# Performance work log

Measured on AMD Instinct MI355X. Metric: run time of the kernel, lower is better.

Reference implementation:

```python
import jax, jax.numpy as jnp
import numpy as np

EPS = 1e-5
NUM_HEADS = 8

def _inorm(x):
    # InstanceNorm1d (affine=False): normalize over last (length) axis per (B, C)
    m = x.mean(axis=-1, keepdims=True)
    v = x.var(axis=-1, keepdims=True)  # biased variance, as torch instance norm
    return (x - m) * jax.lax.rsqrt(v + EPS)

def setup_inputs() -> dict:
    key = jax.random.key(0)
    ks = jax.random.split(key, 12)
    B, Nl, HW = 4, 1024, 4096
    Cl, Cv, Ck, Cval, Cout = 512, 512, 256, 256, 256
    w = lambda k, shape: (jax.random.normal(k, shape, jnp.float32) * 0.02)
    return {
        "l": jax.random.normal(ks[0], (B, Nl, Cl), jnp.float32),
        "x": jax.random.normal(ks[1], (B, HW, Cv), jnp.float32),
        "Wq": w(ks[2], (Ck, Cl)),   "bq": w(ks[3], (Ck,)),
        "Wk": w(ks[4], (Ck, Cv)),   "bk": w(ks[5], (Ck,)),
        "Wv": w(ks[6], (Cval, Cv)), "bv": w(ks[7], (Cval,)),
        "Ww": w(ks[8], (Cout, Cval)), "bw": w(ks[9], (Cout,)),
    }

def reference(l, x, Wq, bq, Wk, bk, Wv, bv, Ww, bw):
    H = NUM_HEADS
    Ck = Wq.shape[0]
    Cv = Wv.shape[0]
    dk, dv = Ck // H, Cv // H
    B, Nl, _ = l.shape
    HW = x.shape[1]

    # 1x1 Conv1d == per-position linear
    q = jnp.einsum('blc,kc->blk', l, Wq) + bq                     # [B, Nl, Ck]
    k = jnp.einsum('bnc,kc->bkn', x, Wk) + bk[None, :, None]      # [B, Ck, HW]
    k = _inorm(k)                                                  # InstanceNorm over HW
    v = jnp.einsum('bnc,kc->bkn', x, Wv) + bv[None, :, None]      # [B, Cv, HW]

    q = q.reshape(B, Nl, H, dk).transpose(0, 2, 1, 3)             # [B, H, Nl, dk]
    k = k.reshape(B, H, dk, HW)                                   # [B, H, dk, HW]
    v = v.reshape(B, H, dv, HW)                                   # [B, H, dv, HW]

    sim = jnp.einsum('bhld,bhdn->bhln', q, k) * (Ck ** -0.5)      # [B, H, Nl, HW]
    att = jax.nn.softmax(sim, axis=-1)
    out = jnp.einsum('bhln,bhdn->bhld', att, v)                   # [B, H, Nl, dv]

    out = out.transpose(0, 2, 1, 3).reshape(B, Nl, Cv)            # [B, Nl, Cv]
    out = jnp.einsum('blc,oc->bol', out, Ww) + bw[None, :, None]  # [B, Cout, Nl]
    out = _inorm(out)                                              # InstanceNorm over Nl
    return out.transpose(0, 2, 1)                                  # [B, Nl, Cout]
```

## Files before the change

kernel.cpp:

```cpp
#include <hip/hip_runtime.h>

constexpr int Bn = 4, NL = 1024, HWn = 4096, NH = 8;

typedef __attribute__((ext_vector_type(8))) short bf16x8;
typedef __attribute__((ext_vector_type(4))) float f32x4;
#define MFMA16 __builtin_amdgcn_mfma_f32_16x16x32_bf16

extern "C" __device__ float __ocml_native_exp2_f32(float);

__device__ __forceinline__ float b2f(unsigned short u) {
  union { unsigned int i; float f; } x; x.i = ((unsigned int)u) << 16; return x.f;
}
__device__ __forceinline__ unsigned short f2b(float f) {
  union { float f; unsigned int i; } x; x.f = f;
  unsigned int r = x.i + 0x7fffu + ((x.i >> 16) & 1u);
  return (unsigned short)(r >> 16);
}

__global__ __launch_bounds__(256) void conv_bf16(const float* __restrict__ src,
    unsigned short* __restrict__ dst, int n)
{
  int i = (blockIdx.x * 256 + threadIdx.x) * 4;
  if (i < n) {
    float4 v = *(const float4*)(src + i);
    ushort4 o; o.x = f2b(v.x); o.y = f2b(v.y); o.z = f2b(v.z); o.w = f2b(v.w);
    *(ushort4*)(dst + i) = o;
  }
}

__global__ __launch_bounds__(256) void conv_w4(const float* __restrict__ Wk,
    const float* __restrict__ Wv, const float* __restrict__ Wq,
    const float* __restrict__ Ww,
    unsigned short* __restrict__ wkb, unsigned short* __restrict__ wvb,
    unsigned short* __restrict__ wqb,
    unsigned short* __restrict__ wwh, unsigned short* __restrict__ wwl)
{
  int i = (blockIdx.x * 256 + threadIdx.x) * 4;
  if (blockIdx.y == 3) {
    if (i >= 65536) return;
    float4 v = *(const float4*)(Ww + i);
    ushort4 hi, lo;
    hi.x = f2b(v.x); lo.x = f2b(v.x - b2f(hi.x));
    hi.y = f2b(v.y); lo.y = f2b(v.y - b2f(hi.y));
    hi.z = f2b(v.z); lo.z = f2b(v.z - b2f(hi.z));
    hi.w = f2b(v.w); lo.w = f2b(v.w - b2f(hi.w));
    *(ushort4*)(wwh + i) = hi;
    *(ushort4*)(wwl + i) = lo;
    return;
  }
  const float* src = blockIdx.y == 0 ? Wk : (blockIdx.y == 1 ? Wv : Wq);
  unsigned short* dst = blockIdx.y == 0 ? wkb : (blockIdx.y == 1 ? wvb : wqb);
  float4 v = *(const float4*)(src + i);
  ushort4 o; o.x = f2b(v.x); o.y = f2b(v.y); o.z = f2b(v.z); o.w = f2b(v.w);
  *(ushort4*)(dst + i) = o;
}

__global__ __launch_bounds__(256, 2) void gemm128(
    const unsigned short* __restrict__ xbf, const unsigned short* __restrict__ lbf,
    const unsigned short* __restrict__ wkb, const unsigned short* __restrict__ wvb,
    const unsigned short* __restrict__ wqb,
    const float* __restrict__ bk, const float* __restrict__ bv, const float* __restrict__ bq,
    unsigned short* __restrict__ khb, unsigned short* __restrict__ vhb,
    unsigned short* __restrict__ qbuf)
{
  __shared__ unsigned short As[2][128 * 32];
  __shared__ unsigned short Bs[2][128 * 32];
  const int id = blockIdx.x;
  const int mode = id < 256 ? 0 : (id < 512 ? 1 : 2);
  const int local = id - (mode == 0 ? 0 : (mode == 1 ? 256 : 512));
  const int rb = local >> 1, cb = local & 1;
  const int m0 = rb * 128, n0 = cb * 128;
  const unsigned short* A = (mode == 2) ? lbf : xbf;
  const unsigned short* W = (mode == 0) ? wkb : (mode == 1 ? wvb : wqb);
  const float* bias = (mode == 0) ? bk : (mode == 1 ? bv : bq);

  const int tid = threadIdx.x, w = tid >> 6, lane = tid & 63;
  const int quad = lane >> 4, l15 = lane & 15;
  const int wr = w >> 1, wc = w & 1;

  const int p0 = tid, p1 = tid + 256;
  const int am0 = p0 >> 2, ak0 = (p0 & 3) * 8;
  const int am1 = p1 >> 2, ak1 = (p1 & 3) * 8;

  f32x4 acc[4][4];
#pragma unroll
  for (int i = 0; i < 4; ++i)
#pragma unroll
    for (int j = 0; j < 4; ++j) acc[i][j] = (f32x4){0.f, 0.f, 0.f, 0.f};

  bf16x8 ar0 = *(const bf16x8*)(A + (size_t)(m0 + am0) * 512 + ak0);
  bf16x8 ar1 = *(const bf16x8*)(A + (size_t)(m0 + am1) * 512 + ak1);
  bf16x8 br0 = *(const bf16x8*)(W + (size_t)(n0 + am0) * 512 + ak0);
  bf16x8 br1 = *(const bf16x8*)(W + (size_t)(n0 + am1) * 512 + ak1);

  for (int kt = 0; kt < 16; ++kt) {
    const int cur = kt & 1;
    *(bf16x8*)&As[cur][p0 * 8] = ar0;
    *(bf16x8*)&As[cur][p1 * 8] = ar1;
    *(bf16x8*)&Bs[cur][p0 * 8] = br0;
    *(bf16x8*)&Bs[cur][p1 * 8] = br1;
    __syncthreads();
    if (kt < 15) {
      int k0 = (kt + 1) * 32;
      ar0 = *(const bf16x8*)(A + (size_t)(m0 + am0) * 512 + k0 + ak0);
      ar1 = *(const bf16x8*)(A + (size_t)(m0 + am1) * 512 + k0 + ak1);
      br0 = *(const bf16x8*)(W + (size_t)(n0 + am0) * 512 + k0 + ak0);
      br1 = *(const bf16x8*)(W + (size_t)(n0 + am1) * 512 + k0 + ak1);
    }
    bf16x8 af[4], bf[4];
#pragma unroll
    for (int fr = 0; fr < 4; ++fr)
      af[fr] = *(const bf16x8*)&As[cur][(wr * 64 + fr * 16 + l15) * 32 + quad * 8];
#pragma unroll
    for (int fc = 0; fc < 4; ++fc)
      bf[fc] = *(const bf16x8*)&Bs[cur][(wc * 64 + fc * 16 + l15) * 32 + quad * 8];
#pragma unroll
    for (int fr = 0; fr < 4; ++fr)
#pragma unroll
      for (int fc = 0; fc < 4; ++fc)
        acc[fr][fc] = MFMA16(af[fr], bf[fc], acc[fr][fc], 0, 0, 0);
  }

  float bb[4];
#pragma unroll
  for (int fc = 0; fc < 4; ++fc) bb[fc] = bias[n0 + wc * 64 + fc * 16 + l15];
  unsigned short* dst = (mode == 0) ? khb : (mode == 1 ? vhb : qbuf);
#pragma unroll
  for (int fr = 0; fr < 4; ++fr) {
#pragma unroll
    for (int fc = 0; fc < 4; ++fc) {
      int col = n0 + wc * 64 + fc * 16 + l15;
#pragma unroll
      for (int r = 0; r < 4; ++r) {
        int row = m0 + wr * 64 + fr * 16 + quad * 4 + r;
        unsigned short val = f2b(acc[fr][fc][r] + bb[fc]);
        if (mode == 2) {
          dst[(size_t)row * 256 + col] = val;
        } else {
          int b = row >> 12, n = row & 4095, h = col >> 5, d = col & 31;
          dst[((size_t)(b * 8 + h) * 4096 + n) * 32 + d] = val;
        }
      }
    }
  }
}

__global__ __launch_bounds__(256) void kvstats(const unsigned short* __restrict__ khb,
    const unsigned short* __restrict__ vhb,
    float* __restrict__ ksum, float* __restrict__ kss, float* __restrict__ vcs)
{
  const int which = blockIdx.x >> 5, bh = blockIdx.x & 31, seg = blockIdx.y;
  const int t = threadIdx.x, d = t & 31, g = t >> 5;
  __shared__ float rs[256], rss[256];
  if (which == 0) {
    const unsigned short* base = khb + (size_t)bh * 131072 + (size_t)seg * 512 * 32;
    float s = 0.f, ss = 0.f;
    for (int i = 0; i < 64; ++i) {
      float v = b2f(base[(size_t)(g + i * 8) * 32 + d]);
      s += v; ss += v * v;
    }
    rs[t] = s; rss[t] = ss;
    __syncthreads();
    if (t < 32) {
      float a = 0.f, b = 0.f;
      for (int g2 = 0; g2 < 8; ++g2) { a += rs[t + g2 * 32]; b += rss[t + g2 * 32]; }
      atomicAdd(&ksum[bh * 32 + t], a);
      atomicAdd(&kss[bh * 32 + t], b);
    }
  } else {
    const unsigned short* base = vhb + (size_t)bh * 131072 + (size_t)seg * 512 * 32;
    float s = 0.f;
    for (int i = 0; i < 64; ++i) s += b2f(base[(size_t)(g + i * 8) * 32 + d]);
    rs[t] = s;
    __syncthreads();
    if (t < 32) {
      float a = 0.f;
      for (int g2 = 0; g2 < 8; ++g2) a += rs[t + g2 * 32];
      vcs[seg * 1024 + bh * 32 + t] = a;
    }
  }
}

__global__ __launch_bounds__(256) void kfinal(const float* __restrict__ ksum,
    const float* __restrict__ kss, float* __restrict__ krstd)
{
  int i = blockIdx.x * 256 + threadIdx.x;
  float m = ksum[i] * (1.f / 4096.f);
  float var = kss[i] * (1.f / 4096.f) - m * m;
  krstd[i] = rsqrtf(var + 1e-5f);
}

__global__ __launch_bounds__(256) void vpack(const unsigned short* __restrict__ vh,
    unsigned short* __restrict__ vfrag)
{
  __shared__ unsigned short vt[256][42];
  const int bh = blockIdx.x >> 4, slab = blockIdx.x & 15;
  const unsigned short* src = vh + ((size_t)bh * 4096 + slab * 256) * 32;
  const int t = threadIdx.x;
#pragma unroll
  for (int i = 0; i < 4; ++i) {
    int p = i * 256 + t;
    int n = p >> 2, piece = p & 3;
    uint4 v = *(const uint4*)(src + (size_t)n * 32 + piece * 8);
    unsigned int* lrow = (unsigned int*)&vt[n][piece * 8];
    lrow[0] = v.x; lrow[1] = v.y; lrow[2] = v.z; lrow[3] = v.w;
  }
  __syncthreads();
#pragma unroll
  for (int i = 0; i < 4; ++i) {
    int op = i * 256 + t;
    int lanep = op & 63, rest = op >> 6;
    int dvt = rest & 1, kh2 = (rest >> 1) & 1, chunkl = rest >> 2;
    int lq = lanep >> 4, ll = lanep & 15;
    unsigned short o[8];
#pragma unroll
    for (int j = 0; j < 8; ++j) {
      int kappa = kh2 * 32 + lq * 8 + j;
      int nloc = (kappa >> 2) + 16 * (kappa & 3);
      o[j] = vt[chunkl * 64 + nloc][dvt * 16 + ll];
    }
    size_t dst = ((((size_t)bh * 64 + slab * 4 + chunkl) * 2 + kh2) * 2 + dvt) * 512 + lanep * 8;
    *(bf16x8*)(vfrag + dst) = *(const bf16x8*)o;
  }
}

__global__ __launch_bounds__(256, 2) void attn5(const unsigned short* __restrict__ qbuf,
    const unsigned short* __restrict__ khb, const unsigned short* __restrict__ vfrag,
    const float* __restrict__ krstd, const float* __restrict__ vcs,
    float* __restrict__ po, float* __restrict__ pd)
{
  const int bh = blockIdx.x, b = bh >> 3, h = bh & 7;
  const int lsuper = blockIdx.y, quarter = blockIdx.z;
  const int tid = threadIdx.x, w = tid >> 6, lane = tid & 63;
  const int quad = lane >> 4, l15 = lane & 15;

  __shared__ unsigned short kb_s[2][2048];
  __shared__ unsigned short vb_s[2][2048];
  __shared__ unsigned short ps[4][4][16][72];

  bf16x8 qa[4];
  {
    float fold[8];
    const float* rp = krstd + bh * 32 + quad * 8;
#pragma unroll
    for (int j = 0; j < 8; ++j) fold[j] = rp[j] * (0.0625f * 1.44269504f);
#pragma unroll
    for (int lf = 0; lf < 4; ++lf) {
      int l = lsuper * 256 + w * 64 + lf * 16 + l15;
      bf16x8 qr = *(const bf16x8*)(qbuf + ((size_t)(b * NL + l)) * 256 + h * 32 + quad * 8);
      const unsigned short* qq = (const unsigned short*)&qr;
      unsigned short tmp[8];
#pragma unroll
      for (int j = 0; j < 8; ++j) tmp[j] = f2b(b2f(qq[j]) * fold[j]);
      qa[lf] = *(const bf16x8*)tmp;
    }
  }

  float drow[4][4];
  f32x4 acc[4][2];
#pragma unroll
  for (int lf = 0; lf < 4; ++lf) {
#pragma unroll
    for (int r = 0; r < 4; ++r) drow[lf][r] = 0.f;
    acc[lf][0] = (f32x4){0.f,0.f,0.f,0.f};
    acc[lf][1] = (f32x4){0.f,0.f,0.f,0.f};
  }

  const unsigned short* kcbase = khb + (size_t)bh * 131072 + (size_t)quarter * 1024 * 32;
  const unsigned short* vcbase = vfrag + (size_t)bh * 131072 + (size_t)quarter * 16 * 2048;

  bf16x8 kreg = *(const bf16x8*)(kcbase + tid * 8);
  bf16x8 vreg = *(const bf16x8*)(vcbase + tid * 8);

  for (int c = 0; c < 16; ++c) {
    const int cur = c & 1;
    *(bf16x8*)&kb_s[cur][tid * 8] = kreg;
    *(bf16x8*)&vb_s[cur][tid * 8] = vreg;
    __syncthreads();
    if (c < 15) {
      kreg = *(const bf16x8*)(kcbase + (c + 1) * 2048 + tid * 8);
      vreg = *(const bf16x8*)(vcbase + (c + 1) * 2048 + tid * 8);
    }

    bf16x8 kb[4];
#pragma unroll
    for (int t = 0; t < 4; ++t)
      kb[t] = *(const bf16x8*)&kb_s[cur][(t * 16 + l15) * 32 + quad * 8];
    bf16x8 vb[4];
#pragma unroll
    for (int i = 0; i < 4; ++i)
      vb[i] = *(const bf16x8*)&vb_s[cur][i * 512 + lane * 8];

    f32x4 z = (f32x4){0.f,0.f,0.f,0.f};
#pragma unroll
    for (int lf = 0; lf < 4; ++lf) {
      f32x4 sv[4];
#pragma unroll
      for (int t = 0; t < 4; ++t) sv[t] = MFMA16(qa[lf], kb[t], z, 0, 0, 0);
#pragma unroll
      for (int r = 0; r < 4; ++r) {
        union { float f; unsigned int u; } e0, e1, e2, e3;
        float x0 = __ocml_native_exp2_f32(sv[0][r]);
        float x1 = __ocml_native_exp2_f32(sv[1][r]);
        float x2 = __ocml_native_exp2_f32(sv[2][r]);
        float x3 = __ocml_native_exp2_f32(sv[3][r]);
        drow[lf][r] += (x0 + x1) + (x2 + x3);
        e0.f = x0 - 1.0f; e1.f = x1 - 1.0f; e2.f = x2 - 1.0f; e3.f = x3 - 1.0f;
        unsigned int lo = (e0.u >> 16) | (e1.u & 0xFFFF0000u);
        unsigned int hi = (e2.u >> 16) | (e3.u & 0xFFFF0000u);
        unsigned int* dst = (unsigned int*)&ps[w][lf][quad * 4 + r][l15 * 4];
        dst[0] = lo; dst[1] = hi;
      }
      asm volatile("s_waitcnt lgkmcnt(0)" ::: "memory");
#pragma unroll
      for (int kh2 = 0; kh2 < 2; ++kh2) {
        bf16x8 pa = *(const bf16x8*)&ps[w][lf][l15][kh2 * 32 + quad * 8];
#pragma unroll
        for (int dvt = 0; dvt < 2; ++dvt)
          acc[lf][dvt] = MFMA16(pa, vb[kh2 * 2 + dvt], acc[lf][dvt], 0, 0, 0);
      }
    }
  }

  const float* vc0 = vcs + (quarter * 2) * 1024 + bh * 32;
  const float* vc1 = vc0 + 1024;
  float cs0 = vc0[l15] + vc1[l15];
  float cs1 = vc0[16 + l15] + vc1[16 + l15];
#pragma unroll
  for (int lf = 0; lf < 4; ++lf)
#pragma unroll
    for (int r = 0; r < 4; ++r) {
      acc[lf][0][r] += cs0;
      acc[lf][1][r] += cs1;
    }

  const size_t PDo = (size_t)quarter * 32768 + (size_t)bh * 1024;
#pragma unroll
  for (int lf = 0; lf < 4; ++lf) {
#pragma unroll
    for (int r = 0; r < 4; ++r) {
      float sv = drow[lf][r];
      sv += __shfl_xor(sv, 1, 16);
      sv += __shfl_xor(sv, 2, 16);
      sv += __shfl_xor(sv, 4, 16);
      sv += __shfl_xor(sv, 8, 16);
      int l = lsuper * 256 + w * 64 + lf * 16 + quad * 4 + r;
      float2 val; val.x = acc[lf][0][r]; val.y = acc[lf][1][r];
      *(float2*)(po + (PDo + l) * 32 + l15 * 2) = val;
      if (l15 == 0) pd[PDo + l] = sv;
    }
  }
}

__global__ __launch_bounds__(256) void combine4(const float* __restrict__ po,
    const float* __restrict__ pd, unsigned short* __restrict__ aoh,
    unsigned short* __restrict__ aol)
{
  int gid = blockIdx.x * 256 + threadIdx.x;
  int dv = gid & 31, l = (gid >> 5) & (NL - 1), h = (gid >> 15) & 7, b = gid >> 18;
  int c = ((dv & 15) << 1) | (dv >> 4);
  size_t r = ((size_t)(b * 8 + h)) * 1024 + l;
  float d = 0.f, o = 0.f;
#pragma unroll
  for (int q = 0; q < 4; ++q) {
    size_t rr = (size_t)q * 32768 + r;
    d += pd[rr];
    o += po[rr * 32 + c];
  }
  o = o / d;
  unsigned short hi = f2b(o);
  size_t idx = ((size_t)(b * NL) + l) * 256 + h * 32 + dv;
  aoh[idx] = hi;
  aol[idx] = f2b(o - b2f(hi));
}

__global__ __launch_bounds__(256) void gemm_proj(
    const unsigned short* __restrict__ aoh, const unsigned short* __restrict__ aol,
    const unsigned short* __restrict__ wwh, const unsigned short* __restrict__ wwl,
    const float* __restrict__ bw, float* __restrict__ pj)
{
  __shared__ unsigned short As[64 * 32];
  __shared__ unsigned short Bs[128 * 32];
  const int bm = blockIdx.x * 64, bn = blockIdx.y * 128;
  const int tid = threadIdx.x, w = tid >> 6, lane = tid & 63;
  const int quad = lane >> 4, l15 = lane & 15;
  const int wr = w >> 1, wc = w & 1;
  const int arow = tid >> 2, apiece = (tid & 3) * 8;

  f32x4 acc[2][4];
#pragma unroll
  for (int i = 0; i < 2; ++i)
#pragma unroll
    for (int j = 0; j < 4; ++j) acc[i][j] = (f32x4){0.f, 0.f, 0.f, 0.f};

  for (int pair = 0; pair < 3; ++pair) {
    const unsigned short* A = (pair == 1) ? aol : aoh;
    const unsigned short* Bm = (pair == 2) ? wwl : wwh;
    for (int kt = 0; kt < 8; ++kt) {
      int k0 = kt * 32;
      __syncthreads();
      *(bf16x8*)&As[tid * 8] = *(const bf16x8*)(A + (size_t)(bm + arow) * 256 + k0 + apiece);
#pragma unroll
      for (int it = 0; it < 2; ++it) {
        int p = tid + it * 256;
        int brow = p >> 2, bpiece = (p & 3) * 8;
        *(bf16x8*)&Bs[p * 8] = *(const bf16x8*)(Bm + (size_t)(bn + brow) * 256 + k0 + bpiece);
      }
      __syncthreads();
      bf16x8 af[2], bf[4];
#pragma unroll
      for (int fr = 0; fr < 2; ++fr)
        af[fr] = *(const bf16x8*)&As[(wr * 32 + fr * 16 + l15) * 32 + quad * 8];
#pragma unroll
      for (int fc = 0; fc < 4; ++fc)
        bf[fc] = *(const bf16x8*)&Bs[(wc * 64 + fc * 16 + l15) * 32 + quad * 8];
#pragma unroll
      for (int fr = 0; fr < 2; ++fr)
#pragma unroll
        for (int fc = 0; fc < 4; ++fc)
          acc[fr][fc] = MFMA16(af[fr], bf[fc], acc[fr][fc], 0, 0, 0);
    }
  }

#pragma unroll
  for (int fr = 0; fr < 2; ++fr)
#pragma unroll
    for (int fc = 0; fc < 4; ++fc) {
      int col = bn + wc * 64 + fc * 16 + l15;
      float bb = bw[col];
#pragma unroll
      for (int r = 0; r < 4; ++r) {
        int row = bm + wr * 32 + fr * 16 + quad * 4 + r;
        pj[(size_t)row * 256 + col] = acc[fr][fc][r] + bb;
      }
    }
}

__global__ __launch_bounds__(256) void stats_kernel(const float* __restrict__ X,
    long batchStride, int rowsPerBlock,
    float* __restrict__ sum, float* __restrict__ sumsq)
{
  const int b = blockIdx.x, c = threadIdx.x;
  const long r0 = (long)blockIdx.y * rowsPerBlock;
  const float* base = X + (long)b * batchStride + r0 * 256 + c;
  float s = 0.f, ss = 0.f;
  for (int r = 0; r < rowsPerBlock; ++r) {
    float v = base[(long)r * 256];
    s += v; ss += v * v;
  }
  atomicAdd(&sum[b * 256 + c], s);
  atomicAdd(&sumsq[b * 256 + c], ss);
}

__global__ __launch_bounds__(256) void finalize_stats(const float* __restrict__ sum,
    const float* __restrict__ sumsq, float invR,
    float* __restrict__ mean, float* __restrict__ rstd)
{
  int i = blockIdx.x * 256 + threadIdx.x;
  float m = sum[i] * invR;
  float v = sumsq[i] * invR - m * m;
  mean[i] = m;
  rstd[i] = rsqrtf(v + 1e-5f);
}

__global__ __launch_bounds__(256) void final_out(const float* __restrict__ proj,
    const float* __restrict__ mean, const float* __restrict__ rstd,
    float* __restrict__ out)
{
  const int b = blockIdx.x, o = threadIdx.x;
  const int l1 = blockIdx.y * 16;
  const float m = mean[b * 256 + o], r = rstd[b * 256 + o];
  for (int i = 0; i < 16; ++i) {
    size_t idx = ((size_t)(b * NL + l1 + i)) * 256 + o;
    out[idx] = (proj[idx] - m) * r;
  }
}

extern "C" void kernel_launch(void* const* d_in, const int* in_sizes, int n_in,
                              void* d_out, int out_size, void* d_ws, size_t ws_size,
                              hipStream_t stream)
{
  const float* l  = (const float*)d_in[0];
  const float* x  = (const float*)d_in[1];
  const float* Wq = (const float*)d_in[2];
  const float* bq = (const float*)d_in[3];
  const float* Wk = (const float*)d_in[4];
  const float* bk = (const float*)d_in[5];
  const float* Wv = (const float*)d_in[6];
  const float* bv = (const float*)d_in[7];
  const float* Ww = (const float*)d_in[8];
  const float* bw = (const float*)d_in[9];
  float* out = (float*)d_out;

  unsigned short* up = (unsigned short*)d_ws;
  unsigned short* xbf   = up;
  unsigned short* lbf   = xbf   + 8388608;
  unsigned short* wkb   = lbf   + 2097152;
  unsigned short* wvb   = wkb   + 131072;
  unsigned short* wqb   = wvb   + 131072;
  unsigned short* qbuf  = wqb   + 131072;
  unsigned short* khb   = qbuf  + 1048576;
  unsigned short* vhb   = khb   + 4194304;
  unsigned short* vfrag = vhb   + 4194304;
  unsigned short* aoh   = vfrag + 4194304;
  unsigned short* aol   = aoh   + 1048576;
  unsigned short* wwh   = aol   + 1048576;
  unsigned short* wwl   = wwh   + 65536;
  float* F     = (float*)((char*)d_ws + 53477376);
  float* krstd = F;
  float* vcs   = krstd + 1024;
  float* po    = vcs + 8192;
  float* pd    = po + 4194304;
  float* pj    = pd + 131072;
  float* st    = pj + 1048576;
  float* ksum  = st;          float* kss   = st + 1024;
  float* psum  = st + 2048;   float* psq   = st + 3072;
  float* pmean = st + 4096;   float* prstd = st + 5120;

  hipMemsetAsync(st, 0, 4096 * sizeof(float), stream);

  dim3 blk(256);
  conv_bf16<<<8192, blk, 0, stream>>>(x,  xbf, 8388608);
  conv_bf16<<<2048, blk, 0, stream>>>(l,  lbf, 2097152);
  conv_w4<<<dim3(128, 4), blk, 0, stream>>>(Wk, Wv, Wq, Ww, wkb, wvb, wqb, wwh, wwl);
  gemm128<<<576, blk, 0, stream>>>(xbf, lbf, wkb, wvb, wqb, bk, bv, bq, khb, vhb, qbuf);
  kvstats<<<dim3(64, 8), blk, 0, stream>>>(khb, vhb, ksum, kss, vcs);
  kfinal<<<4, blk, 0, stream>>>(ksum, kss, krstd);
  vpack<<<512, blk, 0, stream>>>(vhb, vfrag);
  attn5<<<dim3(32, 4, 4), blk, 0, stream>>>(qbuf, khb, vfrag, krstd, vcs, po, pd);
  combine4<<<4096, blk, 0, stream>>>(po, pd, aoh, aol);
  gemm_proj<<<dim3(64, 2), blk, 0, stream>>>(aoh, aol, wwh, wwl, bw, pj);
  stats_kernel<<<dim3(4, 64), blk, 0, stream>>>(pj, (long)NL * 256, 16, psum, psq);
  finalize_stats<<<4, blk, 0, stream>>>(psum, psq, 1.0f / NL, pmean, prstd);
  final_out<<<dim3(4, 64), blk, 0, stream>>>(pj, pmean, prstd, out);
}
```

Baseline: 204.3 us.

## Use direct global-to-LDS async loads and halve attention rows per block

Replaces register-staged global loads plus LDS stores with global_load_lds async copies in both the QKV GEMM and attention kernels. The attention kernel now covers 32 query rows per wave instead of 64, launching twice as many blocks with fewer registers, and occupancy hints are raised. This aims to cut VGPR pressure and LDS store instructions and to improve latency hiding. In exchange, each K/V tile is reloaded by twice as many blocks. There is also no explicit vmcnt wait before the barrier, so correctness depends on the compiler inserting one.

Result: no change. 203.7 us (-0.3%).

```diff
diff --git a/kernel.cpp b/kernel.cpp
--- a/kernel.cpp
+++ b/kernel.cpp
@@ -15,6 +15,12 @@
   union { float f; unsigned int i; } x; x.f = f;
   unsigned int r = x.i + 0x7fffu + ((x.i >> 16) & 1u);
   return (unsigned short)(r >> 16);
+}
+
+__device__ __forceinline__ void async_load16(const unsigned short* g, unsigned short* l) {
+  __builtin_amdgcn_global_load_lds(
+      (const __attribute__((address_space(1))) unsigned int*)g,
+      (__attribute__((address_space(3))) unsigned int*)l, 16, 0, 0);
 }
 
 __global__ __launch_bounds__(256) void conv_bf16(const float* __restrict__ src,
@@ -55,7 +61,7 @@
   *(ushort4*)(dst + i) = o;
 }
 
-__global__ __launch_bounds__(256, 2) void gemm128(
+__global__ __launch_bounds__(256, 3) void gemm128(
     const unsigned short* __restrict__ xbf, const unsigned short* __restrict__ lbf,
     const unsigned short* __restrict__ wkb, const unsigned short* __restrict__ wvb,
     const unsigned short* __restrict__ wqb,
@@ -63,8 +69,8 @@
     unsigned short* __restrict__ khb, unsigned short* __restrict__ vhb,
     unsigned short* __restrict__ qbuf)
 {
-  __shared__ unsigned short As[2][128 * 32];
-  __shared__ unsigned short Bs[2][128 * 32];
+  __shared__ unsigned short As[2][4096];
+  __shared__ unsigned short Bs[2][4096];
   const int id = blockIdx.x;
   const int mode = id < 256 ? 0 : (id < 512 ? 1 : 2);
   const int local = id - (mode == 0 ? 0 : (mode == 1 ? 256 : 512));
@@ -88,24 +94,20 @@
 #pragma unroll
     for (int j = 0; j < 4; ++j) acc[i][j] = (f32x4){0.f, 0.f, 0.f, 0.f};
 
-  bf16x8 ar0 = *(const bf16x8*)(A + (size_t)(m0 + am0) * 512 + ak0);
-  bf16x8 ar1 = *(const bf16x8*)(A + (size_t)(m0 + am1) * 512 + ak1);
-  bf16x8 br0 = *(const bf16x8*)(W + (size_t)(n0 + am0) * 512 + ak0);
-  bf16x8 br1 = *(const bf16x8*)(W + (size_t)(n0 + am1) * 512 + ak1);
+  async_load16(A + (size_t)(m0 + am0) * 512 + ak0, &As[0][p0 * 8]);
+  async_load16(A + (size_t)(m0 + am1) * 512 + ak1, &As[0][p1 * 8]);
+  async_load16(W + (size_t)(n0 + am0) * 512 + ak0, &Bs[0][p0 * 8]);
+  async_load16(W + (size_t)(n0 + am1) * 512 + ak1, &Bs[0][p1 * 8]);
 
   for (int kt = 0; kt < 16; ++kt) {
     const int cur = kt & 1;
-    *(bf16x8*)&As[cur][p0 * 8] = ar0;
-    *(bf16x8*)&As[cur][p1 * 8] = ar1;
-    *(bf16x8*)&Bs[cur][p0 * 8] = br0;
-    *(bf16x8*)&Bs[cur][p1 * 8] = br1;
     __syncthreads();
     if (kt < 15) {
       int k0 = (kt + 1) * 32;
-      ar0 = *(const bf16x8*)(A + (size_t)(m0 + am0) * 512 + k0 + ak0);
-      ar1 = *(const bf16x8*)(A + (size_t)(m0 + am1) * 512 + k0 + ak1);
-      br0 = *(const bf16x8*)(W + (size_t)(n0 + am0) * 512 + k0 + ak0);
-      br1 = *(const bf16x8*)(W + (size_t)(n0 + am1) * 512 + k0 + ak1);
+      async_load16(A + (size_t)(m0 + am0) * 512 + k0 + ak0, &As[cur ^ 1][p0 * 8]);
+      async_load16(A + (size_t)(m0 + am1) * 512 + k0 + ak1, &As[cur ^ 1][p1 * 8]);
+      async_load16(W + (size_t)(n0 + am0) * 512 + k0 + ak0, &Bs[cur ^ 1][p0 * 8]);
+      async_load16(W + (size_t)(n0 + am1) * 512 + k0 + ak1, &Bs[cur ^ 1][p1 * 8]);
     }
     bf16x8 af[4], bf[4];
 #pragma unroll
@@ -224,7 +226,7 @@
   }
 }
 
-__global__ __launch_bounds__(256, 2) void attn5(const unsigned short* __restrict__ qbuf,
+__global__ __launch_bounds__(256, 4) void attn6(const unsigned short* __restrict__ qbuf,
     const unsigned short* __restrict__ khb, const unsigned short* __restrict__ vfrag,
     const float* __restrict__ krstd, const float* __restrict__ vcs,
     float* __restrict__ po, float* __restrict__ pd)
@@ -236,17 +238,17 @@
 
   __shared__ unsigned short kb_s[2][2048];
   __shared__ unsigned short vb_s[2][2048];
-  __shared__ unsigned short ps[4][4][16][72];
-
-  bf16x8 qa[4];
+  __shared__ unsigned short ps[4][2][16][72];
+
+  bf16x8 qa[2];
   {
     float fold[8];
     const float* rp = krstd + bh * 32 + quad * 8;
 #pragma unroll
     for (int j = 0; j < 8; ++j) fold[j] = rp[j] * (0.0625f * 1.44269504f);
 #pragma unroll
-    for (int lf = 0; lf < 4; ++lf) {
-      int l = lsuper * 256 + w * 64 + lf * 16 + l15;
+    for (int lf = 0; lf < 2; ++lf) {
+      int l = lsuper * 128 + w * 32 + lf * 16 + l15;
       bf16x8 qr = *(const bf16x8*)(qbuf + ((size_t)(b * NL + l)) * 256 + h * 32 + quad * 8);
       const unsigned short* qq = (const unsigned short*)&qr;
       unsigned short tmp[8];
@@ -256,10 +258,10 @@
     }
   }
 
-  float drow[4][4];
-  f32x4 acc[4][2];
-#pragma unroll
-  for (int lf = 0; lf < 4; ++lf) {
+  float drow[2][4];
+  f32x4 acc[2][2];
+#pragma unroll
+  for (int lf = 0; lf < 2; ++lf) {
 #pragma unroll
     for (int r = 0; r < 4; ++r) drow[lf][r] = 0.f;
     acc[lf][0] = (f32x4){0.f,0.f,0.f,0.f};
@@ -269,17 +271,15 @@
   const unsigned short* kcbase = khb + (size_t)bh * 131072 + (size_t)quarter * 1024 * 32;
   const unsigned short* vcbase = vfrag + (size_t)bh * 131072 + (size_t)quarter * 16 * 2048;
 
-  bf16x8 kreg = *(const bf16x8*)(kcbase + tid * 8);
-  bf16x8 vreg = *(const bf16x8*)(vcbase + tid * 8);
+  async_load16(kcbase + tid * 8, &kb_s[0][tid * 8]);
+  async_load16(vcbase + tid * 8, &vb_s[0][tid * 8]);
 
   for (int c = 0; c < 16; ++c) {
     const int cur = c & 1;
-    *(bf16x8*)&kb_s[cur][tid * 8] = kreg;
-    *(bf16x8*)&vb_s[cur][tid * 8] = vreg;
     __syncthreads();
     if (c < 15) {
-      kreg = *(const bf16x8*)(kcbase + (c + 1) * 2048 + tid * 8);
-      vreg = *(const bf16x8*)(vcbase + (c + 1) * 2048 + tid * 8);
+      async_load16(kcbase + (c + 1) * 2048 + tid * 8, &kb_s[cur ^ 1][tid * 8]);
+      async_load16(vcbase + (c + 1) * 2048 + tid * 8, &vb_s[cur ^ 1][tid * 8]);
     }
 
     bf16x8 kb[4];
@@ -293,7 +293,7 @@
 
     f32x4 z = (f32x4){0.f,0.f,0.f,0.f};
 #pragma unroll
-    for (int lf = 0; lf < 4; ++lf) {
+    for (int lf = 0; lf < 2; ++lf) {
       f32x4 sv[4];
 #pragma unroll
       for (int t = 0; t < 4; ++t) sv[t] = MFMA16(qa[lf], kb[t], z, 0, 0, 0);
@@ -306,10 +306,10 @@
         float x3 = __ocml_native_exp2_f32(sv[3][r]);
         drow[lf][r] += (x0 + x1) + (x2 + x3);
         e0.f = x0 - 1.0f; e1.f = x1 - 1.0f; e2.f = x2 - 1.0f; e3.f = x3 - 1.0f;
-        unsigned int lo = (e0.u >> 16) | (e1.u & 0xFFFF0000u);
-        unsigned int hi = (e2.u >> 16) | (e3.u & 0xFFFF0000u);
-        unsigned int* dst = (unsigned int*)&ps[w][lf][quad * 4 + r][l15 * 4];
-        dst[0] = lo; dst[1] = hi;
+        uint2 pk;
+        pk.x = (e0.u >> 16) | (e1.u & 0xFFFF0000u);
+        pk.y = (e2.u >> 16) | (e3.u & 0xFFFF0000u);
+        *(uint2*)&ps[w][lf][quad * 4 + r][l15 * 4] = pk;
       }
       asm volatile("s_waitcnt lgkmcnt(0)" ::: "memory");
 #pragma unroll
@@ -327,7 +327,7 @@
   float cs0 = vc0[l15] + vc1[l15];
   float cs1 = vc0[16 + l15] + vc1[16 + l15];
 #pragma unroll
-  for (int lf = 0; lf < 4; ++lf)
+  for (int lf = 0; lf < 2; ++lf)
 #pragma unroll
     for (int r = 0; r < 4; ++r) {
       acc[lf][0][r] += cs0;
@@ -336,7 +336,7 @@
 
   const size_t PDo = (size_t)quarter * 32768 + (size_t)bh * 1024;
 #pragma unroll
-  for (int lf = 0; lf < 4; ++lf) {
+  for (int lf = 0; lf < 2; ++lf) {
 #pragma unroll
     for (int r = 0; r < 4; ++r) {
       float sv = drow[lf][r];
@@ -344,7 +344,7 @@
       sv += __shfl_xor(sv, 2, 16);
       sv += __shfl_xor(sv, 4, 16);
       sv += __shfl_xor(sv, 8, 16);
-      int l = lsuper * 256 + w * 64 + lf * 16 + quad * 4 + r;
+      int l = lsuper * 128 + w * 32 + lf * 16 + quad * 4 + r;
       float2 val; val.x = acc[lf][0][r]; val.y = acc[lf][1][r];
       *(float2*)(po + (PDo + l) * 32 + l15 * 2) = val;
       if (l15 == 0) pd[PDo + l] = sv;
@@ -527,7 +527,7 @@
   kvstats<<<dim3(64, 8), blk, 0, stream>>>(khb, vhb, ksum, kss, vcs);
   kfinal<<<4, blk, 0, stream>>>(ksum, kss, krstd);
   vpack<<<512, blk, 0, stream>>>(vhb, vfrag);
-  attn5<<<dim3(32, 4, 4), blk, 0, stream>>>(qbuf, khb, vfrag, krstd, vcs, po, pd);
+  attn6<<<dim3(32, 8, 4), blk, 0, stream>>>(qbuf, khb, vfrag, krstd, vcs, po, pd);
   combine4<<<4096, blk, 0, stream>>>(po, pd, aoh, aol);
   gemm_proj<<<dim3(64, 2), blk, 0, stream>>>(aoh, aol, wwh, wwl, bw, pj);
   stats_kernel<<<dim3(4, 64), blk, 0, stream>>>(pj, (long)NL * 256, 16, psum, psq);
```
